# Performance work log

Hardware: AMD Instinct MI355X
Metric: run time of the kernel (lower is better)

Reference implementation:

```python
import jax, jax.numpy as jnp
import numpy as np

NA, NB = 120001, 260001   # atoms+1, directed bonds+1 (row 0 = padding)
ATOM_FDIM, BOND_FDIM, H, MAX_NB = 133, 147, 256, 6


def setup_inputs() -> dict:
    key = jax.random.key(0)
    ks = jax.random.split(key, 9)
    f_atoms = jax.random.normal(ks[0], (NA, ATOM_FDIM), dtype=jnp.float32)
    f_bonds = jax.random.normal(ks[1], (NB, BOND_FDIM), dtype=jnp.float32)
    # padding row 0 is all-zero features (SimpleBatchGraph prepends zeros)
    f_atoms = f_atoms.at[0].set(0.0)
    f_bonds = f_bonds.at[0].set(0.0)
    a2b = jax.random.randint(ks[2], (NA, MAX_NB), 0, NB)
    b2a = jax.random.randint(ks[3], (NB,), 0, NA)
    b2revb = jax.random.randint(ks[4], (NB,), 0, NB)
    W_i = jax.random.normal(ks[5], (BOND_FDIM, H), dtype=jnp.float32) * 0.05
    W_h = jax.random.normal(ks[6], (H, H), dtype=jnp.float32) * 0.05
    W_o = jax.random.normal(ks[7], (ATOM_FDIM + H, H), dtype=jnp.float32) * 0.05
    b_o = jax.random.normal(ks[8], (H,), dtype=jnp.float32) * 0.05
    return {
        "f_atoms": f_atoms, "f_bonds": f_bonds,
        "a2b": a2b, "b2a": b2a, "b2revb": b2revb,
        "W_i": W_i, "W_h": W_h, "W_o": W_o, "b_o": b_o,
        "depth": 3, "n_mols": 6000, "atoms_per_mol": 20,
    }


def reference(f_atoms, f_bonds, a2b, b2a, b2revb, W_i, W_h, W_o, b_o,
              depth, n_mols, atoms_per_mol):
    # D-MPNN bond-message passing (atom_messages=False, dropout=0, ReLU, mean agg)
    inp = f_bonds @ W_i                      # [NB, H]  (no bias)
    message = jax.nn.relu(inp)
    for _ in range(depth - 1):
        nei = message[a2b]                   # [NA, MAX_NB, H] gather
        a_message = nei.sum(axis=1)          # [NA, H]
        message = a_message[b2a] - message[b2revb]   # [NB, H]
        message = jax.nn.relu(inp + message @ W_h)
    a_message = message[a2b].sum(axis=1)     # [NA, H]
    a_input = jnp.concatenate([f_atoms, a_message], axis=1)   # [NA, ATOM_FDIM+H]
    atom_hiddens = jax.nn.relu(a_input @ W_o + b_o)           # [NA, H]
    # a_scope: contiguous equal-size molecules after dropping padding row 0
    mol_vecs = atom_hiddens[1:].reshape(n_mols, atoms_per_mol, -1).mean(axis=1)
    return mol_vecs
```

## Files before the change

kernel.cpp:

```cpp
#include <hip/hip_runtime.h>


#define DI __device__ __forceinline__

typedef __bf16 bf16x8 __attribute__((ext_vector_type(8)));
typedef float f32x8 __attribute__((ext_vector_type(8)));
typedef float f32x16 __attribute__((ext_vector_type(16)));
typedef unsigned short u16x8 __attribute__((ext_vector_type(8)));

static constexpr int cNA = 120001;
static constexpr int cNB = 260001;
static constexpr int cAF = 133;
static constexpr int cBF = 147;
static constexpr int KP_F = 160;

DI bf16x8 ldbf8(const unsigned short* p) {
  return __builtin_bit_cast(bf16x8, *reinterpret_cast<const u16x8*>(p));
}
DI void stbf8(unsigned short* p, bf16x8 v) {
  *reinterpret_cast<u16x8*>(p) = __builtin_bit_cast(u16x8, v);
}
DI f32x8 up8(bf16x8 v) { return __builtin_convertvector(v, f32x8); }
DI f32x8 up8u(u16x8 v) { return up8(__builtin_bit_cast(bf16x8, v)); }
DI bf16x8 dn8(f32x8 v) { return __builtin_convertvector(v, bf16x8); }
DI float bfh2f(unsigned short h) { return __builtin_bit_cast(float, (unsigned)h << 16); }
DI unsigned short f2bfh(float f) {
  __bf16 b = (__bf16)f;
  return __builtin_bit_cast(unsigned short, b);
}

__global__ void k_padcvt8(const float* __restrict__ in, unsigned short* __restrict__ out,
                          int nrows, int kin, int kpad) {
  long long total = (long long)nrows * (kpad / 8);
  long long i = (long long)blockIdx.x * blockDim.x + threadIdx.x;
  if (i >= total) return;
  int row = (int)(i / (kpad / 8));
  int k0 = (int)(i - (long long)row * (kpad / 8)) * 8;
  const float* src = in + (long long)row * kin;
  f32x8 v;
#pragma unroll
  for (int e = 0; e < 8; e++) v[e] = (k0 + e < kin) ? src[k0 + e] : 0.f;
  stbf8(out + (long long)row * kpad + k0, dn8(v));
}

__global__ void k_transw(const float* __restrict__ W, unsigned short* __restrict__ out,
                         int K, int kpad, int rowoff) {
  int i = blockIdx.x * blockDim.x + threadIdx.x;
  if (i >= 256 * kpad) return;
  int n = i / kpad, k = i - n * kpad;
  float v = (k < K) ? W[(long long)(k + rowoff) * 256 + n] : 0.f;
  out[i] = f2bfh(v);
}

__global__ __launch_bounds__(256) void k_gathersum(
    const unsigned short* __restrict__ src, const int* __restrict__ a2b,
    unsigned short* __restrict__ out, int relu_flag) {
  int tid = blockIdx.x * 256 + threadIdx.x;
  if (tid >= cNA * 16) return;
  int atom = tid >> 4, ch = tid & 15;
  const int* ab = a2b + (long long)atom * 6;
  int bidx[6];
#pragma unroll
  for (int j = 0; j < 6; j++) bidx[j] = ab[j];
  u16x8 r0[6], r1[6];
#pragma unroll
  for (int j = 0; j < 6; j++) {
    const unsigned short* p = src + (long long)bidx[j] * 256 + ch * 16;
    r0[j] = *reinterpret_cast<const u16x8*>(p);
    r1[j] = *reinterpret_cast<const u16x8*>(p + 8);
  }
  f32x8 lo = {0.f,0.f,0.f,0.f,0.f,0.f,0.f,0.f}, hi = lo;
#pragma unroll
  for (int j = 0; j < 6; j++) {
    f32x8 x0 = up8u(r0[j]);
    f32x8 x1 = up8u(r1[j]);
    if (relu_flag) {
#pragma unroll
      for (int e = 0; e < 8; e++) { x0[e] = fmaxf(x0[e], 0.f); x1[e] = fmaxf(x1[e], 0.f); }
    }
#pragma unroll
    for (int e = 0; e < 8; e++) { lo[e] += x0[e]; hi[e] += x1[e]; }
  }
  unsigned short* q = out + (long long)atom * 256 + ch * 16;
  stbf8(q, dn8(lo));
  stbf8(q + 8, dn8(hi));
}

enum { MODE_BF16OUT = 0, MODE_MSG = 2, MODE_FINAL = 3 };

template <int KP, int MODE, bool RELU_SRC>
__global__ __launch_bounds__(1024) void k_gemm(
    const unsigned short* __restrict__ A,
    const unsigned short* __restrict__ Msg,
    const int* __restrict__ b2a, const int* __restrict__ b2revb,
    const unsigned short* __restrict__ Wt,
    const unsigned short* __restrict__ Cbf,
    const float* __restrict__ bias,
    unsigned short* __restrict__ OutBf, int nrows) {
  constexpr int NF = KP / 16;
  constexpr int NCB = 8;
  constexpr int NSTAGE = (KP == 256) ? 2 : 1;
  constexpr int CBS = NCB / NSTAGE;
  __shared__ unsigned short lds[CBS * NF * 512];

  const int tid = threadIdx.x;
  const int lane = tid & 63, wid = tid >> 6;
  const int rbase = blockIdx.x * 512 + wid * 32;
  const int rA = rbase + (lane & 31);
  const int rS = rA < nrows ? rA : 0;
  const int kg = lane >> 5;

  bf16x8 af[NF];
  if (MODE == MODE_MSG) {
    int ib = b2a[rS];
    int irv = b2revb[rS];
    const unsigned short* pa = A + (long long)ib * 256;
    const unsigned short* pm = Msg + (long long)irv * 256;
    u16x8 rawa[NF], rawm[NF];
#pragma unroll
    for (int f = 0; f < NF; f++) {
      int off = f * 16 + kg * 8;
      rawa[f] = *reinterpret_cast<const u16x8*>(pa + off);
      rawm[f] = *reinterpret_cast<const u16x8*>(pm + off);
    }
#pragma unroll
    for (int f = 0; f < NF; f++) {
      f32x8 xa = up8u(rawa[f]);
      f32x8 xm = up8u(rawm[f]);
      if (RELU_SRC) {
#pragma unroll
      for (int e = 0; e < 8; e++) xm[e] = fmaxf(xm[e], 0.f);
      }
      af[f] = dn8(xa - xm);
    }
  } else {
    const unsigned short* pa = A + (long long)rS * KP;
#pragma unroll
    for (int f = 0; f < NF; f++) af[f] = ldbf8(pa + f * 16 + kg * 8);
  }

  float bv[NCB];
  if (MODE == MODE_FINAL) {
#pragma unroll
    for (int cb = 0; cb < NCB; cb++) bv[cb] = bias[cb * 32 + (lane & 31)];
  }

#pragma unroll 1
  for (int stage = 0; stage < NSTAGE; stage++) {
    if (stage) __syncthreads();
    for (int c = tid; c < CBS * NF * 64; c += 1024) {
      int frag = c >> 6, slot = c & 63;
      int cb_l = frag / NF, f = frag - cb_l * NF;
      int col = (stage * CBS + cb_l) * 32 + (slot & 31);
      int koff = f * 16 + (slot >> 5) * 8;
      *reinterpret_cast<u16x8*>(lds + c * 8) =
          *reinterpret_cast<const u16x8*>(Wt + (long long)col * KP + koff);
    }
    __syncthreads();

#pragma unroll 1
    for (int cb_l = 0; cb_l < CBS; cb_l++) {
      const int cb = stage * CBS + cb_l;
      const int col = cb * 32 + (lane & 31);
      const int rb2 = rbase + 4 * kg;

      unsigned short craw[16];
      if (MODE == MODE_MSG || MODE == MODE_FINAL) {
#pragma unroll
        for (int q = 0; q < 16; q++) {
          int row = rb2 + (q & 3) + 8 * (q >> 2);
          int rowc = row < nrows ? row : 0;
          craw[q] = Cbf[(long long)rowc * 256 + col];
        }
      }

      f32x16 acc;
#pragma unroll
      for (int q = 0; q < 16; q++) acc[q] = 0.f;
      const unsigned short* lb = lds + cb_l * NF * 512 + lane * 8;
#pragma unroll
      for (int f = 0; f < NF; f++) {
        bf16x8 b = ldbf8(lb + f * 512);
        acc = __builtin_amdgcn_mfma_f32_32x32x16_bf16(af[f], b, acc, 0, 0, 0);
      }

#pragma unroll
      for (int q = 0; q < 16; q++) {
        int row = rb2 + (q & 3) + 8 * (q >> 2);
        if (row >= nrows) continue;
        float v = acc[q];
        long long idx = (long long)row * 256 + col;
        if (MODE == MODE_BF16OUT) {
          OutBf[idx] = f2bfh(v);
        } else if (MODE == MODE_MSG) {
          v += bfh2f(craw[q]);
          v = fmaxf(v, 0.f);
          OutBf[idx] = f2bfh(v);
        } else {
          v += bfh2f(craw[q]) + bv[cb];
          v = fmaxf(v, 0.f);
          OutBf[idx] = f2bfh(v);
        }
      }
    }
  }
}

__global__ __launch_bounds__(256) void k_meanpool(const unsigned short* __restrict__ ah,
                                                  float* __restrict__ out) {
  int m = blockIdx.x, c = threadIdx.x;
  unsigned short r[20];
#pragma unroll
  for (int i = 0; i < 20; i++) r[i] = ah[(long long)(1 + m * 20 + i) * 256 + c];
  float s = 0.f;
#pragma unroll
  for (int i = 0; i < 20; i++) s += bfh2f(r[i]);
  out[(long long)m * 256 + c] = s * 0.05f;
}

extern "C" void kernel_launch(void* const* d_in, const int* in_sizes, int n_in,
                              void* d_out, int out_size, void* d_ws, size_t ws_size,
                              hipStream_t stream) {
  const float* f_atoms = (const float*)d_in[0];
  const float* f_bonds = (const float*)d_in[1];
  const int* a2b = (const int*)d_in[2];
  const int* b2a = (const int*)d_in[3];
  const int* b2revb = (const int*)d_in[4];
  const float* W_i = (const float*)d_in[5];
  const float* W_h = (const float*)d_in[6];
  const float* W_o = (const float*)d_in[7];
  const float* b_o = (const float*)d_in[8];
  float* out = (float*)d_out;

  char* ws = (char*)d_ws;
  size_t off = 0;
  auto alloc = [&](size_t b) { size_t o = off; off += (b + 1023) & ~(size_t)1023; return o; };
  size_t o_fb = alloc((size_t)cNB * KP_F * 2);
  size_t o_fa = alloc((size_t)cNA * KP_F * 2);
  size_t o_inp = alloc((size_t)cNB * 256 * 2);
  size_t o_bufA = alloc((size_t)cNB * 256 * 2);
  size_t o_bufB = alloc((size_t)cNB * 256 * 2);
  size_t o_wti = alloc((size_t)256 * KP_F * 2);
  size_t o_wth = alloc((size_t)256 * 256 * 2);
  size_t o_wo1 = alloc((size_t)256 * KP_F * 2);
  size_t o_wo2 = alloc((size_t)256 * 256 * 2);

  unsigned short* fb16 = (unsigned short*)(ws + o_fb);
  unsigned short* amsg = (unsigned short*)(ws + o_fb);
  unsigned short* fa16 = (unsigned short*)(ws + o_fa);
  unsigned short* inp = (unsigned short*)(ws + o_inp);
  unsigned short* msgA = (unsigned short*)(ws + o_bufA);
  unsigned short* msgB = (unsigned short*)(ws + o_bufB);
  unsigned short* pf = (unsigned short*)(ws + o_bufA);
  unsigned short* ah = (unsigned short*)(ws + o_bufB);
  unsigned short* Wti = (unsigned short*)(ws + o_wti);
  unsigned short* Wth = (unsigned short*)(ws + o_wth);
  unsigned short* Wto1 = (unsigned short*)(ws + o_wo1);
  unsigned short* Wto2 = (unsigned short*)(ws + o_wo2);

  dim3 b256(256);
  {
    long long t = (long long)cNB * (KP_F / 8);
    k_padcvt8<<<(unsigned)((t + 255) / 256), b256, 0, stream>>>(f_bonds, fb16, cNB, cBF, KP_F);
  }
  {
    long long t = (long long)cNA * (KP_F / 8);
    k_padcvt8<<<(unsigned)((t + 255) / 256), b256, 0, stream>>>(f_atoms, fa16, cNA, cAF, KP_F);
  }
  k_transw<<<(256 * KP_F + 255) / 256, b256, 0, stream>>>(W_i, Wti, cBF, KP_F, 0);
  k_transw<<<(256 * 256 + 255) / 256, b256, 0, stream>>>(W_h, Wth, 256, 256, 0);
  k_transw<<<(256 * KP_F + 255) / 256, b256, 0, stream>>>(W_o, Wto1, cAF, KP_F, 0);
  k_transw<<<(256 * 256 + 255) / 256, b256, 0, stream>>>(W_o, Wto2, 256, 256, cAF);

  const int gB = (cNB + 511) / 512;
  const int gA = (cNA + 511) / 512;
  const int gS = (cNA * 16 + 255) / 256;

  k_gemm<KP_F, MODE_BF16OUT, false><<<gB, 1024, 0, stream>>>(
      fb16, nullptr, nullptr, nullptr, Wti, nullptr, nullptr, inp, cNB);
  k_gathersum<<<gS, b256, 0, stream>>>(inp, a2b, amsg, 1);
  k_gemm<256, MODE_MSG, true><<<gB, 1024, 0, stream>>>(
      amsg, inp, b2a, b2revb, Wth, inp, nullptr, msgA, cNB);
  k_gathersum<<<gS, b256, 0, stream>>>(msgA, a2b, amsg, 0);
  k_gemm<256, MODE_MSG, false><<<gB, 1024, 0, stream>>>(
      amsg, msgA, b2a, b2revb, Wth, inp, nullptr, msgB, cNB);
  k_gathersum<<<gS, b256, 0, stream>>>(msgB, a2b, amsg, 0);
  k_gemm<KP_F, MODE_BF16OUT, false><<<gA, 1024, 0, stream>>>(
      fa16, nullptr, nullptr, nullptr, Wto1, nullptr, nullptr, pf, cNA);
  k_gemm<256, MODE_FINAL, false><<<gA, 1024, 0, stream>>>(
      amsg, nullptr, nullptr, nullptr, Wto2, pf, b_o, ah, cNA);
  k_meanpool<<<6000, b256, 0, stream>>>(ah, out);
}
```

Baseline: 1.108 ms.

## Switch GEMM kernels to 16x16x32 MFMA tiles with 256-row blocks

Each wave now works on a 16-row tile using the 16x16x32 bf16 MFMA instead of a 32-row tile with the 32x32x16 MFMA. This halves the A fragments held per lane and changes the LDS weight layout to 16-column tiles, always loaded in two stages. Blocks now cover 256 rows, so the grid doubles, and launch bounds request higher occupancy. The aim is to cut register pressure and raise occupancy to hide gather latency, at the cost of reusing each staged weight tile across fewer rows.

```diff
diff --git a/kernel.cpp b/kernel.cpp
--- a/kernel.cpp
+++ b/kernel.cpp
@@ -4,8 +4,8 @@
 #define DI __device__ __forceinline__
 
 typedef __bf16 bf16x8 __attribute__((ext_vector_type(8)));
+typedef float f32x4 __attribute__((ext_vector_type(4)));
 typedef float f32x8 __attribute__((ext_vector_type(8)));
-typedef float f32x16 __attribute__((ext_vector_type(16)));
 typedef unsigned short u16x8 __attribute__((ext_vector_type(8)));
 
 static constexpr int cNA = 120001;
@@ -89,7 +89,7 @@
 enum { MODE_BF16OUT = 0, MODE_MSG = 2, MODE_FINAL = 3 };
 
 template <int KP, int MODE, bool RELU_SRC>
-__global__ __launch_bounds__(1024) void k_gemm(
+__global__ __launch_bounds__(1024, 8) void k_gemm(
     const unsigned short* __restrict__ A,
     const unsigned short* __restrict__ Msg,
     const int* __restrict__ b2a, const int* __restrict__ b2revb,
@@ -97,18 +97,16 @@
     const unsigned short* __restrict__ Cbf,
     const float* __restrict__ bias,
     unsigned short* __restrict__ OutBf, int nrows) {
-  constexpr int NF = KP / 16;
-  constexpr int NCB = 8;
-  constexpr int NSTAGE = (KP == 256) ? 2 : 1;
-  constexpr int CBS = NCB / NSTAGE;
-  __shared__ unsigned short lds[CBS * NF * 512];
+  constexpr int NF = KP / 32;
+  constexpr int CTS = 8;
+  __shared__ unsigned short lds[CTS * NF * 512];
 
   const int tid = threadIdx.x;
   const int lane = tid & 63, wid = tid >> 6;
-  const int rbase = blockIdx.x * 512 + wid * 32;
-  const int rA = rbase + (lane & 31);
+  const int wrow0 = blockIdx.x * 256 + wid * 16;
+  const int rA = wrow0 + (lane & 15);
   const int rS = rA < nrows ? rA : 0;
-  const int kg = lane >> 5;
+  const int koff = (lane >> 4) * 8;
 
   bf16x8 af[NF];
   if (MODE == MODE_MSG) {
@@ -116,77 +114,74 @@
     int irv = b2revb[rS];
     const unsigned short* pa = A + (long long)ib * 256;
     const unsigned short* pm = Msg + (long long)irv * 256;
-    u16x8 rawa[NF], rawm[NF];
-#pragma unroll
-    for (int f = 0; f < NF; f++) {
-      int off = f * 16 + kg * 8;
-      rawa[f] = *reinterpret_cast<const u16x8*>(pa + off);
-      rawm[f] = *reinterpret_cast<const u16x8*>(pm + off);
-    }
-#pragma unroll
-    for (int f = 0; f < NF; f++) {
-      f32x8 xa = up8u(rawa[f]);
-      f32x8 xm = up8u(rawm[f]);
-      if (RELU_SRC) {
-#pragma unroll
-      for (int e = 0; e < 8; e++) xm[e] = fmaxf(xm[e], 0.f);
-      }
-      af[f] = dn8(xa - xm);
+#pragma unroll
+    for (int h = 0; h < NF / 4; h++) {
+      u16x8 rawa[4], rawm[4];
+#pragma unroll
+      for (int t = 0; t < 4; t++) {
+        int off = (h * 4 + t) * 32 + koff;
+        rawa[t] = *reinterpret_cast<const u16x8*>(pa + off);
+        rawm[t] = *reinterpret_cast<const u16x8*>(pm + off);
+      }
+#pragma unroll
+      for (int t = 0; t < 4; t++) {
+        f32x8 xa = up8u(rawa[t]);
+        f32x8 xm = up8u(rawm[t]);
+        if (RELU_SRC) {
+#pragma unroll
+          for (int e = 0; e < 8; e++) xm[e] = fmaxf(xm[e], 0.f);
+        }
+        af[h * 4 + t] = dn8(xa - xm);
+      }
     }
   } else {
     const unsigned short* pa = A + (long long)rS * KP;
 #pragma unroll
-    for (int f = 0; f < NF; f++) af[f] = ldbf8(pa + f * 16 + kg * 8);
-  }
-
-  float bv[NCB];
-  if (MODE == MODE_FINAL) {
-#pragma unroll
-    for (int cb = 0; cb < NCB; cb++) bv[cb] = bias[cb * 32 + (lane & 31)];
+    for (int f = 0; f < NF; f++) af[f] = ldbf8(pa + f * 32 + koff);
   }
 
 #pragma unroll 1
-  for (int stage = 0; stage < NSTAGE; stage++) {
+  for (int stage = 0; stage < 2; stage++) {
     if (stage) __syncthreads();
-    for (int c = tid; c < CBS * NF * 64; c += 1024) {
+    for (int c = tid; c < CTS * NF * 64; c += 1024) {
       int frag = c >> 6, slot = c & 63;
-      int cb_l = frag / NF, f = frag - cb_l * NF;
-      int col = (stage * CBS + cb_l) * 32 + (slot & 31);
-      int koff = f * 16 + (slot >> 5) * 8;
+      int ctl = frag / NF, f = frag - ctl * NF;
+      int col = stage * 128 + ctl * 16 + (slot & 15);
+      int ko = f * 32 + (slot >> 4) * 8;
       *reinterpret_cast<u16x8*>(lds + c * 8) =
-          *reinterpret_cast<const u16x8*>(Wt + (long long)col * KP + koff);
+          *reinterpret_cast<const u16x8*>(Wt + (long long)col * KP + ko);
     }
     __syncthreads();
 
 #pragma unroll 1
-    for (int cb_l = 0; cb_l < CBS; cb_l++) {
-      const int cb = stage * CBS + cb_l;
-      const int col = cb * 32 + (lane & 31);
-      const int rb2 = rbase + 4 * kg;
-
-      unsigned short craw[16];
+    for (int ctl = 0; ctl < CTS; ctl++) {
+      const int ct = stage * CTS + ctl;
+      const int col = ct * 16 + (lane & 15);
+      const int r0 = wrow0 + (lane >> 4) * 4;
+
+      unsigned short craw[4];
       if (MODE == MODE_MSG || MODE == MODE_FINAL) {
 #pragma unroll
-        for (int q = 0; q < 16; q++) {
-          int row = rb2 + (q & 3) + 8 * (q >> 2);
+        for (int q = 0; q < 4; q++) {
+          int row = r0 + q;
           int rowc = row < nrows ? row : 0;
           craw[q] = Cbf[(long long)rowc * 256 + col];
         }
       }
-
-      f32x16 acc;
-#pragma unroll
-      for (int q = 0; q < 16; q++) acc[q] = 0.f;
-      const unsigned short* lb = lds + cb_l * NF * 512 + lane * 8;
+      float bvv = 0.f;
+      if (MODE == MODE_FINAL) bvv = bias[col];
+
+      f32x4 acc = {0.f, 0.f, 0.f, 0.f};
+      const unsigned short* lb = lds + ctl * NF * 512 + lane * 8;
 #pragma unroll
       for (int f = 0; f < NF; f++) {
         bf16x8 b = ldbf8(lb + f * 512);
-        acc = __builtin_amdgcn_mfma_f32_32x32x16_bf16(af[f], b, acc, 0, 0, 0);
-      }
-
-#pragma unroll
-      for (int q = 0; q < 16; q++) {
-        int row = rb2 + (q & 3) + 8 * (q >> 2);
+        acc = __builtin_amdgcn_mfma_f32_16x16x32_bf16(af[f], b, acc, 0, 0, 0);
+      }
+
+#pragma unroll
+      for (int q = 0; q < 4; q++) {
+        int row = r0 + q;
         if (row >= nrows) continue;
         float v = acc[q];
         long long idx = (long long)row * 256 + col;
@@ -197,7 +192,7 @@
           v = fmaxf(v, 0.f);
           OutBf[idx] = f2bfh(v);
         } else {
-          v += bfh2f(craw[q]) + bv[cb];
+          v += bfh2f(craw[q]) + bvv;
           v = fmaxf(v, 0.f);
           OutBf[idx] = f2bfh(v);
         }
@@ -272,8 +267,8 @@
   k_transw<<<(256 * KP_F + 255) / 256, b256, 0, stream>>>(W_o, Wto1, cAF, KP_F, 0);
   k_transw<<<(256 * 256 + 255) / 256, b256, 0, stream>>>(W_o, Wto2, 256, 256, cAF);
 
-  const int gB = (cNB + 511) / 512;
-  const int gA = (cNA + 511) / 512;
+  const int gB = (cNB + 255) / 256;
+  const int gA = (cNA + 255) / 256;
   const int gS = (cNA * 16 + 255) / 256;
 
   k_gemm<KP_F, MODE_BF16OUT, false><<<gB, 1024, 0, stream>>>(
```

Measured after the change: 941.2 us. -15.0%, faster.
